# Kernel tuning notes

Hardware: AMD Instinct MI355X
Metric: run time of the kernel (lower is better)

The kernel has to match this reference:

```python
import jax, jax.numpy as jnp
import numpy as np

N, E = 3072, 49152
C_IN, HID, C_OUT = 16, 64, 3
KS = (2000, 1000, 500)  # ceil(pool_ratio * n_nodes) per depth: 2000/3072, 0.5, 0.5


def gcn(x, A, W, b):
    # GCNConv(improved=True) with edge weights: A_hat = A + 2I,
    # out = D^-1/2 A_hat D^-1/2 (x W) + b
    n = A.shape[0]
    i = jnp.arange(n)
    A_hat = A.at[i, i].add(2.0)
    deg = A_hat.sum(axis=1)
    dis = jnp.where(deg > 0, 1.0 / jnp.sqrt(deg), 0.0)
    return (dis[:, None] * A_hat * dis[None, :]) @ (x @ W) + b


def augment(A):
    # GraphUNet.augment_adj: remove self loops, add self loops (w=1),
    # spspmm(A, A) -> A^2, remove self loops. Dense equivalent.
    n = A.shape[0]
    i = jnp.arange(n)
    A1 = A.at[i, i].set(1.0)
    A2 = A1 @ A1
    return A2.at[i, i].set(0.0)


def topk_pool(x, A, p, k):
    # TopKPooling: score = tanh((x . p)/||p||), keep top-k nodes, scale features
    score = jnp.tanh((x @ p) / jnp.linalg.norm(p))
    _, perm = jax.lax.top_k(score, k)
    x = x[perm] * score[perm][:, None]
    return x, A[perm][:, perm], perm


def setup_inputs():
    key = jax.random.key(0)
    ks = jax.random.split(key, 16)
    g = lambda k, shape, s=1.0: jax.random.normal(k, shape, dtype=jnp.float32) * s
    s = 0.1
    return {
        "x": g(ks[0], (N, C_IN)),
        "edge_index": jax.random.randint(ks[1], (2, E), 0, N),
        "Wd0": g(ks[2], (C_IN, HID), s), "bd0": jnp.zeros((HID,), jnp.float32),
        "Wd1": g(ks[3], (HID, HID), s), "bd1": jnp.zeros((HID,), jnp.float32),
        "Wd2": g(ks[4], (HID, HID), s), "bd2": jnp.zeros((HID,), jnp.float32),
        "Wd3": g(ks[5], (HID, HID), s), "bd3": jnp.zeros((HID,), jnp.float32),
        "p1": g(ks[6], (HID,), s), "p2": g(ks[7], (HID,), s), "p3": g(ks[8], (HID,), s),
        "Wu0": g(ks[9], (HID, HID), s), "bu0": jnp.zeros((HID,), jnp.float32),
        "Wu1": g(ks[10], (HID, HID), s), "bu1": jnp.zeros((HID,), jnp.float32),
        "Wu2": g(ks[11], (HID, C_OUT), s), "bu2": jnp.zeros((C_OUT,), jnp.float32),
    }


def reference(x, edge_index, Wd0, bd0, Wd1, bd1, Wd2, bd2, Wd3, bd3,
              p1, p2, p3, Wu0, bu0, Wu1, bu1, Wu2, bu2):
    # eval mode: dropout_edge(p=0.2) and F.dropout(p=0.92) are identity
    # dense weighted adjacency; duplicate edges sum, matching sparse scatter-add
    A = jnp.zeros((N, N), jnp.float32).at[edge_index[0], edge_index[1]].add(1.0)
    x = jax.nn.relu(gcn(x, A, Wd0, bd0))
    xs, adjs, perms = [x], [A], []
    for i, (W, b, p) in enumerate(((Wd1, bd1, p1), (Wd2, bd2, p2), (Wd3, bd3, p3))):
        A = augment(A)
        x, A, perm = topk_pool(x, A, p, KS[i])
        x = jax.nn.relu(gcn(x, A, W, b))
        if i < 2:
            xs.append(x)
            adjs.append(A)
        perms.append(perm)
    for i, (W, b) in enumerate(((Wu0, bu0), (Wu1, bu1), (Wu2, bu2))):
        j = 2 - i
        res, Aj, perm = xs[j], adjs[j], perms[j]
        up = jnp.zeros_like(res).at[perm].set(x)  # unpool
        x = gcn(res + up, Aj, W, b)  # sum_res=True skip connection
        if i < 2:
            x = jax.nn.relu(x)
    return jax.nn.softmax(x, axis=1)
```

## Files before the change

### kernel.cpp

```cpp
#include <hip/hip_runtime.h>
#include <hip/hip_bf16.h>
#include <cstdint>
#include <cstddef>
#include <math.h>


#define DIVUP(a,b) (((a)+(b)-1)/(b))

using s16x8 = __attribute__((ext_vector_type(8))) short;
using f32x4 = __attribute__((ext_vector_type(4))) float;

__device__ __forceinline__ unsigned short f2bf(float v) {
    union { float f; unsigned u; } a; a.f = v;
    unsigned u = a.u;
    u = u + 0x7FFFu + ((u >> 16) & 1u);
    return (unsigned short)(u >> 16);
}
__device__ __forceinline__ float bf2f(unsigned short h) {
    union { unsigned u; float f; } a; a.u = ((unsigned)h) << 16; return a.f;
}
__device__ __forceinline__ void gload_lds16(const unsigned short* g, unsigned short* l) {
    __builtin_amdgcn_global_load_lds(
        (const __attribute__((address_space(1))) void*)g,
        (__attribute__((address_space(3))) void*)l, 16, 0, 0);
}


__global__ void k_scatter(const int* __restrict__ e, float* __restrict__ A, int E, int n) {
    int t = blockIdx.x * blockDim.x + threadIdx.x;
    if (t < E) atomicAdd(&A[(size_t)e[t] * n + e[E + t]], 1.0f);
}

__global__ void k_a0_plane(const float* __restrict__ A, unsigned short* __restrict__ H,
                           float* __restrict__ d0, float* __restrict__ dsum, int n) {
    int t = blockIdx.x * 256 + threadIdx.x;
    int i = t / n, j = t - i * n;
    float v = A[t];
    if (i == j) { d0[i] = v; v = 1.0f; }
    H[t] = f2bf(v);
    __shared__ float red[256];
    red[threadIdx.x] = v; __syncthreads();
    for (int o = 128; o > 0; o >>= 1) {
        if (threadIdx.x < o) red[threadIdx.x] += red[threadIdx.x + o];
        __syncthreads();
    }
    if (threadIdx.x == 0) atomicAdd(&dsum[i], red[0]);
}

__global__ void k_transpose_bf(const unsigned short* __restrict__ S, unsigned short* __restrict__ D, int n) {
    __shared__ unsigned short tile[32][33];
    int bx = blockIdx.x * 32, by = blockIdx.y * 32;
    #pragma unroll
    for (int dy = 0; dy < 32; dy += 8)
        tile[threadIdx.y + dy][threadIdx.x] = S[(size_t)(by + threadIdx.y + dy) * n + bx + threadIdx.x];
    __syncthreads();
    #pragma unroll
    for (int dy = 0; dy < 32; dy += 8)
        D[(size_t)(bx + threadIdx.y + dy) * n + by + threadIdx.x] = tile[threadIdx.x][threadIdx.y + dy];
}

__global__ void k_disv(const float* __restrict__ dsum, const float* __restrict__ diag,
                       float* __restrict__ dis, int n) {
    int i = blockIdx.x * blockDim.x + threadIdx.x;
    if (i >= n) return;
    float deg = dsum[i] + 1.0f + (diag ? diag[i] : 0.0f);
    dis[i] = deg > 0.f ? 1.0f / sqrtf(deg) : 0.f;
}

__global__ void k_scores(const float* __restrict__ x, const float* __restrict__ pv,
                         float* __restrict__ sc, int n) {
    __shared__ float pl[64];
    if (threadIdx.x < 64) pl[threadIdx.x] = pv[threadIdx.x];
    __syncthreads();
    float n2 = 0.f;
    #pragma unroll
    for (int k = 0; k < 64; ++k) n2 += pl[k] * pl[k];
    float nrm = sqrtf(n2);
    int i = blockIdx.x * blockDim.x + threadIdx.x;
    if (i >= n) return;
    const float* xr = x + (size_t)i * 64;
    float d = 0.f;
    #pragma unroll
    for (int k = 0; k < 64; ++k) d += xr[k] * pl[k];
    sc[i] = tanhf(d / nrm);
}

__global__ void k_count_rank(const float* __restrict__ score, int* __restrict__ rank, int n) {
    __shared__ float ls[256];
    const int i = blockIdx.x * 256 + threadIdx.x;
    const int j0 = blockIdx.y * 256;
    int jj_n = n - j0; if (jj_n > 256) jj_n = 256;
    ls[threadIdx.x] = (j0 + threadIdx.x < n) ? score[j0 + threadIdx.x] : -INFINITY;
    __syncthreads();
    if (i >= n) return;
    const float si = score[i];
    int cnt = 0;
    for (int jj = 0; jj < jj_n; ++jj) {
        float sj = ls[jj];
        int j = j0 + jj;
        cnt += (sj > si) || (sj == si && j < i);
    }
    atomicAdd(&rank[i], cnt);
}

__global__ void k_scatter_topk(const float* __restrict__ score, const int* __restrict__ rank,
                               int n, int k, int kp, int* __restrict__ perm, float* __restrict__ scout) {
    int i = blockIdx.x * blockDim.x + threadIdx.x;
    if (i < n) {
        int r = rank[i];
        if (r < k) { perm[r] = i; scout[r] = score[i]; }
    }
    if (i >= k && i < kp) { perm[i] = 0; scout[i] = 0.f; }
}

__global__ void k_pool_x(const float* __restrict__ x, const int* __restrict__ perm,
                         const float* __restrict__ sc, float* __restrict__ xo, int k) {
    int t = blockIdx.x * blockDim.x + threadIdx.x;
    if (t >= k * 64) return;
    int r = t >> 6;
    xo[t] = x[(size_t)perm[r] * 64 + (t & 63)] * sc[r];
}

__global__ void k_copy4(const float4* __restrict__ src, float4* __restrict__ dst, int n4) {
    int t = blockIdx.x * blockDim.x + threadIdx.x;
    if (t < n4) dst[t] = src[t];
}

__global__ void k_scatter_rows(const float* __restrict__ xc, const int* __restrict__ perm,
                               float* __restrict__ o, int k) {
    int t = blockIdx.x * blockDim.x + threadIdx.x;
    if (t >= k * 64) return;
    int r = t >> 6;
    o[(size_t)perm[r] * 64 + (t & 63)] += xc[t];
}

__global__ void k_xw(const float* __restrict__ x, const float* __restrict__ W,
                     const float* __restrict__ dis, int n, int np, int cin, int ldw, int nout,
                     float* __restrict__ Y, unsigned short* __restrict__ T0,
                     unsigned short* __restrict__ T1, unsigned short* __restrict__ T2) {
    int t = blockIdx.x * blockDim.x + threadIdx.x;
    if (t >= np * 64) return;
    int i = t >> 6, f = t & 63;
    float y = 0.f;
    if (i < n && f < nout) {
        float a = 0.f;
        for (int k = 0; k < cin; ++k) a += x[(size_t)i * cin + k] * W[(size_t)k * ldw + f];
        y = dis[i] * a;
    }
    Y[t] = y;
    unsigned short h0 = f2bf(y);
    float r1 = y - bf2f(h0);
    unsigned short h1 = f2bf(r1);
    float r2 = r1 - bf2f(h1);
    size_t ti = (size_t)f * np + i;
    T0[ti] = h0; T1[ti] = h1; T2[ti] = f2bf(r2);
}


template<int PA, int PB, int ATOMIC>
__global__ __launch_bounds__(256) void k_aug_gemm(
    const unsigned short* __restrict__ Pa, const unsigned short* __restrict__ Pb,
    const unsigned short* __restrict__ Qa, const unsigned short* __restrict__ Qb,
    const int* __restrict__ perm, int M, int N, int kchunk, int ns, float* __restrict__ C)
{
    __shared__ __align__(16) unsigned short lp[PA * 8192];
    __shared__ __align__(16) unsigned short lq[PB * 8192];
    const int tid = threadIdx.x, lane = tid & 63;
    const int wm = tid >> 7, wn = (tid >> 6) & 1;
    const int bm = blockIdx.x * 128, bn = blockIdx.y * 128;
    const int kbeg = blockIdx.z * kchunk;
    const unsigned short* P[2] = {Pa, Pb};
    const unsigned short* Q[2] = {Qa, Qb};
    const unsigned short* sp[PA][4];
    const unsigned short* sq[PB][4];
    int dst[4];
    #pragma unroll
    for (int it = 0; it < 4; ++it) {
        int s = tid + it * 256;
        int row = s >> 3, c = (s & 7) ^ (row & 7);
        dst[it] = (s - lane) * 8;
        #pragma unroll
        for (int p = 0; p < PA; ++p)
            sp[p][it] = P[p] + (size_t)perm[bm + row] * ns + kbeg + 8 * c;
        #pragma unroll
        for (int p = 0; p < PB; ++p)
            sq[p][it] = Q[p] + (size_t)perm[bn + row] * ns + kbeg + 8 * c;
    }
    f32x4 acc[4][4] = {};
    const int l15 = lane & 15, kb = lane >> 4;
    const int nt = kchunk >> 6;

    for (int tt = 0; tt < nt; ++tt) {
        if (tt) __syncthreads();
        int koff = tt * 64;
        #pragma unroll
        for (int p = 0; p < PA; ++p)
            #pragma unroll
            for (int it = 0; it < 4; ++it)
                gload_lds16(sp[p][it] + koff, &lp[p * 8192 + dst[it]]);
        #pragma unroll
        for (int p = 0; p < PB; ++p)
            #pragma unroll
            for (int it = 0; it < 4; ++it)
                gload_lds16(sq[p][it] + koff, &lq[p * 8192 + dst[it]]);
        __syncthreads();
        #pragma unroll
        for (int h = 0; h < 2; ++h) {
            s16x8 av[PA][4], bv[PB][4];
            #pragma unroll
            for (int p = 0; p < PA; ++p)
                #pragma unroll
                for (int mi = 0; mi < 4; ++mi) {
                    int row = wm * 64 + mi * 16 + l15;
                    int slot = (h * 4 + kb) ^ (row & 7);
                    av[p][mi] = *(const s16x8*)&lp[p * 8192 + row * 64 + slot * 8];
                }
            #pragma unroll
            for (int p = 0; p < PB; ++p)
                #pragma unroll
                for (int ni = 0; ni < 4; ++ni) {
                    int row = wn * 64 + ni * 16 + l15;
                    int slot = (h * 4 + kb) ^ (row & 7);
                    bv[p][ni] = *(const s16x8*)&lq[p * 8192 + row * 64 + slot * 8];
                }
            #pragma unroll
            for (int mi = 0; mi < 4; ++mi)
                #pragma unroll
                for (int ni = 0; ni < 4; ++ni)
                    #pragma unroll
                    for (int pa = 0; pa < PA; ++pa)
                        #pragma unroll
                        for (int pb = 0; pb < PB; ++pb)
                            acc[mi][ni] = __builtin_amdgcn_mfma_f32_16x16x32_bf16(
                                av[pa][mi], bv[pb][ni], acc[mi][ni], 0, 0, 0);
        }
    }

    const int l4 = lane >> 4;
    for (int mi = 0; mi < 4; ++mi)
        for (int ni = 0; ni < 4; ++ni)
            #pragma unroll
            for (int r = 0; r < 4; ++r) {
                int row = bm + wm * 64 + mi * 16 + l4 * 4 + r;
                int col = bn + wn * 64 + ni * 16 + l15;
                if (row < M && col < N) {
                    float v = acc[mi][ni][r];
                    if (ATOMIC) { if (v != 0.f) atomicAdd(&C[(size_t)row * N + col], v); }
                    else C[(size_t)row * N + col] = v;
                }
            }
}

template<int PA>
__global__ __launch_bounds__(256) void k_gcn_gemm(
    const unsigned short* __restrict__ Aa, const unsigned short* __restrict__ Ab,
    const unsigned short* __restrict__ Ac,
    const unsigned short* __restrict__ B0, const unsigned short* __restrict__ B1,
    const unsigned short* __restrict__ B2,
    int np, int kchunk, float* __restrict__ Zp)
{
    __shared__ __align__(16) unsigned short la[PA * 4096];
    __shared__ __align__(16) unsigned short lb[3 * 4096];
    const int tid = threadIdx.x, lane = tid & 63, wv = tid >> 6;
    const int bm = blockIdx.x * 64;
    const int kbeg = blockIdx.y * kchunk;
    const unsigned short* A[3] = {Aa, Ab, Ac};
    const unsigned short* B[3] = {B0, B1, B2};
    const unsigned short* sa[PA][2];
    const unsigned short* sb[3][2];
    int dst[2];
    #pragma unroll
    for (int it = 0; it < 2; ++it) {
        int s = tid + it * 256;
        int row = s >> 3, c = (s & 7) ^ (row & 7);
        dst[it] = (s - lane) * 8;
        #pragma unroll
        for (int p = 0; p < PA; ++p)
            sa[p][it] = A[p] + (size_t)(bm + row) * np + kbeg + 8 * c;
        #pragma unroll
        for (int p = 0; p < 3; ++p)
            sb[p][it] = B[p] + (size_t)row * np + kbeg + 8 * c;
    }
    f32x4 acc[4] = {};
    const int l15 = lane & 15, kb = lane >> 4;
    const int nt = kchunk >> 6;

    for (int tt = 0; tt < nt; ++tt) {
        if (tt) __syncthreads();
        int koff = tt * 64;
        #pragma unroll
        for (int p = 0; p < PA; ++p)
            #pragma unroll
            for (int it = 0; it < 2; ++it)
                gload_lds16(sa[p][it] + koff, &la[p * 4096 + dst[it]]);
        #pragma unroll
        for (int p = 0; p < 3; ++p)
            #pragma unroll
            for (int it = 0; it < 2; ++it)
                gload_lds16(sb[p][it] + koff, &lb[p * 4096 + dst[it]]);
        __syncthreads();
        #pragma unroll
        for (int h = 0; h < 2; ++h) {
            s16x8 av[PA], bv[3][4];
            #pragma unroll
            for (int p = 0; p < PA; ++p) {
                int row = wv * 16 + l15;
                int slot = (h * 4 + kb) ^ (row & 7);
                av[p] = *(const s16x8*)&la[p * 4096 + row * 64 + slot * 8];
            }
            #pragma unroll
            for (int p = 0; p < 3; ++p)
                #pragma unroll
                for (int ni = 0; ni < 4; ++ni) {
                    int row = ni * 16 + l15;
                    int slot = (h * 4 + kb) ^ (row & 7);
                    bv[p][ni] = *(const s16x8*)&lb[p * 4096 + row * 64 + slot * 8];
                }
            #pragma unroll
            for (int ni = 0; ni < 4; ++ni)
                #pragma unroll
                for (int pa = 0; pa < PA; ++pa)
                    #pragma unroll
                    for (int pb = 0; pb <= 2 - pa; ++pb)
                        acc[ni] = __builtin_amdgcn_mfma_f32_16x16x32_bf16(
                            av[pa], bv[pb][ni], acc[ni], 0, 0, 0);
        }
    }

    const int l4 = lane >> 4;
    float* Z = Zp + (size_t)blockIdx.y * np * 64;
    for (int ni = 0; ni < 4; ++ni)
        #pragma unroll
        for (int r = 0; r < 4; ++r) {
            int row = bm + wv * 16 + l4 * 4 + r;
            Z[(size_t)row * 64 + ni * 16 + l15] = acc[ni][r];
        }
}

__global__ void k_gcn_epi(const float* __restrict__ Zp, const float* __restrict__ Y,
                          const float* __restrict__ dis, const float* __restrict__ diagv,
                          const float* __restrict__ b, int n, int np, int nout, int relu,
                          float* __restrict__ xo) {
    int t = blockIdx.x * blockDim.x + threadIdx.x;
    if (t >= n * 64) return;
    int i = t >> 6, f = t & 63;
    float s = 0.f;
    for (int kq = 0; kq < 8; ++kq) s += Zp[(size_t)kq * np * 64 + t];
    float coef = 1.f + (diagv ? diagv[i] : 0.f);
    float v = dis[i] * (s + coef * Y[t]) + (f < nout ? b[f] : 0.f);
    if (relu) v = fmaxf(v, 0.f);
    xo[t] = v;
}

template<int NP, int NT>
__global__ void k_split_t(const float* __restrict__ C, int kk, int kp,
                          unsigned short* __restrict__ H0, unsigned short* __restrict__ H1,
                          unsigned short* __restrict__ H2,
                          unsigned short* __restrict__ T0, unsigned short* __restrict__ T1,
                          float* __restrict__ dsum) {
    __shared__ unsigned short tl[NT ? NT : 1][32][33];
    const int tx = threadIdx.x & 31, ty = threadIdx.x >> 5;
    const int r0 = blockIdx.y * 32, c0 = blockIdx.x * 32;
    const int c = c0 + tx;
    #pragma unroll
    for (int dy = 0; dy < 4; ++dy) {
        int rt = ty + dy * 8;
        int r = r0 + rt;
        float v = 0.f;
        if (r < kk && c < kk) v = (r == c) ? 1.f : C[(size_t)r * kk + c];
        unsigned short h0 = f2bf(v);
        size_t o = (size_t)r * kp + c;
        H0[o] = h0;
        if (NT > 0) tl[0][rt][tx] = h0;
        if (NP > 1) {
            float r1 = v - bf2f(h0);
            unsigned short h1 = f2bf(r1);
            H1[o] = h1;
            if (NT > 1) tl[1][rt][tx] = h1;
            if (NP > 2) H2[o] = f2bf(r1 - bf2f(h1));
        }
        float sum = v;
        #pragma unroll
        for (int o2 = 16; o2 > 0; o2 >>= 1) sum += __shfl_xor(sum, o2, 32);
        if (tx == 0) atomicAdd(&dsum[r], sum);
    }
    if (NT > 0) {
        __syncthreads();
        #pragma unroll
        for (int dy = 0; dy < 4; ++dy) {
            int rt = ty + dy * 8;
            size_t o = (size_t)(c0 + rt) * kp + r0 + tx;
            T0[o] = tl[0][tx][rt];
            if (NT > 1) T1[o] = tl[1][tx][rt];
        }
    }
}

__global__ void k_softmax(const float* __restrict__ lg, float* __restrict__ o, int n) {
    int i = blockIdx.x * blockDim.x + threadIdx.x;
    if (i >= n) return;
    float a = lg[i * 64], b = lg[i * 64 + 1], c = lg[i * 64 + 2];
    float m = fmaxf(a, fmaxf(b, c));
    float ea = expf(a - m), eb = expf(b - m), ec = expf(c - m);
    float s = ea + eb + ec;
    o[i * 3] = ea / s; o[i * 3 + 1] = eb / s; o[i * 3 + 2] = ec / s;
}


extern "C" void kernel_launch(void* const* d_in, const int* in_sizes, int n_in,
                              void* d_out, int out_size, void* d_ws, size_t ws_size,
                              hipStream_t stream) {
    const int N0 = 3072;
    const int E = in_sizes[1] / 2;
    const int CIN = in_sizes[0] / N0;

    const float* x_in = (const float*)d_in[0];
    const int*   eidx = (const int*)d_in[1];
    const float* Wd0 = (const float*)d_in[2];  const float* bd0 = (const float*)d_in[3];
    const float* Wd1 = (const float*)d_in[4];  const float* bd1 = (const float*)d_in[5];
    const float* Wd2 = (const float*)d_in[6];  const float* bd2 = (const float*)d_in[7];
    const float* Wd3 = (const float*)d_in[8];  const float* bd3 = (const float*)d_in[9];
    const float* p1  = (const float*)d_in[10]; const float* p2  = (const float*)d_in[11];
    const float* p3  = (const float*)d_in[12];
    const float* Wu0 = (const float*)d_in[13]; const float* bu0 = (const float*)d_in[14];
    const float* Wu1 = (const float*)d_in[15]; const float* bu1 = (const float*)d_in[16];
    const float* Wu2 = (const float*)d_in[17]; const float* bu2 = (const float*)d_in[18];
    float* out = (float*)d_out;

    char* ws = (char*)d_ws;
    size_t off = 0;
    auto alloc = [&](size_t bytes) -> void* {
        off = (off + 255) & ~(size_t)255;
        void* p = ws + off;
        off += bytes;
        return p;
    };

    unsigned short* A0H  = (unsigned short*)alloc((size_t)3072 * 3072 * 2);
    unsigned short* A0T  = (unsigned short*)alloc((size_t)3072 * 3072 * 2);
    float* d0   = (float*)alloc(3072 * 4);
    float* dis0 = (float*)alloc(3072 * 4);
    float* x0   = (float*)alloc((size_t)3072 * 64 * 4);
    unsigned short* P1H = (unsigned short*)alloc((size_t)2048 * 2048 * 2);
    unsigned short* P1T = (unsigned short*)alloc((size_t)2048 * 2048 * 2);
    float* dis1 = (float*)alloc(2048 * 4);
    float* x1   = (float*)alloc((size_t)2048 * 64 * 4);
    float* xp1  = (float*)alloc((size_t)2048 * 64 * 4);
    unsigned short* P2H  = (unsigned short*)alloc((size_t)1024 * 1024 * 2);
    unsigned short* P2L  = (unsigned short*)alloc((size_t)1024 * 1024 * 2);
    unsigned short* P2TH = (unsigned short*)alloc((size_t)1024 * 1024 * 2);
    unsigned short* P2TL = (unsigned short*)alloc((size_t)1024 * 1024 * 2);
    float* dis2 = (float*)alloc(1024 * 4);
    float* x2   = (float*)alloc((size_t)1024 * 64 * 4);
    float* xp2  = (float*)alloc((size_t)1024 * 64 * 4);
    unsigned short* P3a = (unsigned short*)alloc((size_t)512 * 512 * 2);
    unsigned short* P3b = (unsigned short*)alloc((size_t)512 * 512 * 2);
    unsigned short* P3c = (unsigned short*)alloc((size_t)512 * 512 * 2);
    float* dis3 = (float*)alloc(512 * 4);
    float* x3   = (float*)alloc((size_t)512 * 64 * 4);
    float* xp3  = (float*)alloc((size_t)512 * 64 * 4);
    int*   perm1 = (int*)alloc(2048 * 4);  float* sc1 = (float*)alloc(2048 * 4);
    int*   perm2 = (int*)alloc(1024 * 4);  float* sc2 = (float*)alloc(1024 * 4);
    int*   perm3 = (int*)alloc(512 * 4);   float* sc3 = (float*)alloc(512 * 4);
    float* score = (float*)alloc(3072 * 4);
    float* dsum0 = (float*)alloc(3072 * 4);
    float* dsum1 = (float*)alloc(2048 * 4);
    float* dsum2 = (float*)alloc(1024 * 4);
    float* dsum3 = (float*)alloc(512 * 4);
    int* rank1 = (int*)alloc(3072 * 4);
    int* rank2 = (int*)alloc(2048 * 4);
    int* rank3 = (int*)alloc(1024 * 4);
    float* Yf  = (float*)alloc((size_t)3072 * 64 * 4);
    unsigned short* Yt0 = (unsigned short*)alloc((size_t)64 * 3072 * 2);
    unsigned short* Yt1 = (unsigned short*)alloc((size_t)64 * 3072 * 2);
    unsigned short* Yt2 = (unsigned short*)alloc((size_t)64 * 3072 * 2);
    float* Zp   = (float*)alloc((size_t)8 * 3072 * 64 * 4);
    float* xlog = (float*)alloc((size_t)3072 * 64 * 4);
    float* t2b  = (float*)alloc((size_t)1024 * 64 * 4);
    float* t1b  = (float*)alloc((size_t)2048 * 64 * 4);
    float* t0b  = (float*)alloc((size_t)3072 * 64 * 4);
    char* scratch = (char*)alloc((size_t)3072 * 3072 * 4);
    if (off > ws_size) return;

    float* A0f = (float*)scratch;
    float* C1  = (float*)scratch;
    float* C2  = (float*)scratch;
    float* C3  = (float*)scratch;

    auto gcn = [&](const float* xin, int cin, const float* W, int ldw, int nout, const float* bias,
                   const unsigned short* Pa, const unsigned short* Pb2, const unsigned short* Pc,
                   int PA, int n, int np2, const float* dis, const float* diagv, int relu, float* xout) {
        k_xw<<<DIVUP(np2 * 64, 256), 256, 0, stream>>>(xin, W, dis, n, np2, cin, ldw, nout, Yf, Yt0, Yt1, Yt2);
        dim3 gg(np2 / 64, 8);
        int kch = np2 / 8;
        if (PA == 1)      k_gcn_gemm<1><<<gg, 256, 0, stream>>>(Pa, Pa, Pa, Yt0, Yt1, Yt2, np2, kch, Zp);
        else if (PA == 2) k_gcn_gemm<2><<<gg, 256, 0, stream>>>(Pa, Pb2, Pb2, Yt0, Yt1, Yt2, np2, kch, Zp);
        else              k_gcn_gemm<3><<<gg, 256, 0, stream>>>(Pa, Pb2, Pc, Yt0, Yt1, Yt2, np2, kch, Zp);
        k_gcn_epi<<<DIVUP(n * 64, 256), 256, 0, stream>>>(Zp, Yf, dis, diagv, bias, n, np2, nout, relu, xout);
    };

    auto topk = [&](const float* x, const float* pvec, int n, int k, int kp,
                    int* rank, int* perm, float* scv) {
        k_scores<<<DIVUP(n, 256), 256, 0, stream>>>(x, pvec, score, n);
        dim3 gr(DIVUP(n, 256), DIVUP(n, 256));
        k_count_rank<<<gr, 256, 0, stream>>>(score, rank, n);
        k_scatter_topk<<<DIVUP(n, 256), 256, 0, stream>>>(score, rank, n, k, kp, perm, scv);
    };

    hipMemsetAsync(dsum0, 0, (char*)(rank3 + 1024) - (char*)dsum0, stream);

    hipMemsetAsync(A0f, 0, (size_t)3072 * 3072 * 4, stream);
    k_scatter<<<DIVUP(E, 256), 256, 0, stream>>>(eidx, A0f, E, N0);
    k_a0_plane<<<3072 * 3072 / 256, 256, 0, stream>>>(A0f, A0H, d0, dsum0, N0);
    k_transpose_bf<<<dim3(96, 96), dim3(32, 8), 0, stream>>>(A0H, A0T, 3072);
    k_disv<<<DIVUP(3072, 256), 256, 0, stream>>>(dsum0, d0, dis0, 3072);

    gcn(x_in, CIN, Wd0, 64, 64, bd0, A0H, A0H, A0H, 1, 3072, 3072, dis0, d0, 1, x0);

    topk(x0, p1, 3072, 2000, 2048, rank1, perm1, sc1);
    k_pool_x<<<DIVUP(2000 * 64, 256), 256, 0, stream>>>(x0, perm1, sc1, xp1, 2000);
    hipMemsetAsync(C1, 0, (size_t)2000 * 2000 * 4, stream);
    k_aug_gemm<1, 1, 1><<<dim3(16, 16, 8), 256, 0, stream>>>(A0H, A0H, A0T, A0T, perm1, 2000, 2000, 384, 3072, C1);
    k_split_t<1, 1><<<dim3(64, 64), 256, 0, stream>>>(C1, 2000, 2048, P1H, P1H, P1H, P1T, P1T, dsum1);
    k_disv<<<DIVUP(2048, 256), 256, 0, stream>>>(dsum1, nullptr, dis1, 2048);
    gcn(xp1, 64, Wd1, 64, 64, bd1, P1H, P1H, P1H, 1, 2000, 2048, dis1, nullptr, 1, x1);

    topk(x1, p2, 2000, 1000, 1024, rank2, perm2, sc2);
    k_pool_x<<<DIVUP(1000 * 64, 256), 256, 0, stream>>>(x1, perm2, sc2, xp2, 1000);
    hipMemsetAsync(C2, 0, (size_t)1000 * 1000 * 4, stream);
    k_aug_gemm<1, 1, 1><<<dim3(8, 8, 8), 256, 0, stream>>>(P1H, P1H, P1T, P1T, perm2, 1000, 1000, 256, 2048, C2);
    k_split_t<2, 2><<<dim3(32, 32), 256, 0, stream>>>(C2, 1000, 1024, P2H, P2L, P2L, P2TH, P2TL, dsum2);
    k_disv<<<DIVUP(1024, 256), 256, 0, stream>>>(dsum2, nullptr, dis2, 1024);
    gcn(xp2, 64, Wd2, 64, 64, bd2, P2H, P2L, P2L, 2, 1000, 1024, dis2, nullptr, 1, x2);

    topk(x2, p3, 1000, 500, 512, rank3, perm3, sc3);
    k_pool_x<<<DIVUP(500 * 64, 256), 256, 0, stream>>>(x2, perm3, sc3, xp3, 500);
    hipMemsetAsync(C3, 0, (size_t)500 * 500 * 4, stream);
    k_aug_gemm<2, 2, 1><<<dim3(4, 4, 16), 256, 0, stream>>>(P2H, P2L, P2TH, P2TL, perm3, 500, 500, 64, 1024, C3);
    k_split_t<3, 0><<<dim3(16, 16), 256, 0, stream>>>(C3, 500, 512, P3a, P3b, P3c, nullptr, nullptr, dsum3);
    k_disv<<<DIVUP(512, 256), 256, 0, stream>>>(dsum3, nullptr, dis3, 512);
    gcn(xp3, 64, Wd3, 64, 64, bd3, P3a, P3b, P3c, 3, 500, 512, dis3, nullptr, 1, x3);

    k_copy4<<<DIVUP(1000 * 16, 256), 256, 0, stream>>>((const float4*)x2, (float4*)t2b, 1000 * 16);
    k_scatter_rows<<<DIVUP(500 * 64, 256), 256, 0, stream>>>(x3, perm3, t2b, 500);
    gcn(t2b, 64, Wu0, 64, 64, bu0, P2H, P2L, P2L, 2, 1000, 1024, dis2, nullptr, 1, xp2);

    k_copy4<<<DIVUP(2000 * 16, 256), 256, 0, stream>>>((const float4*)x1, (float4*)t1b, 2000 * 16);
    k_scatter_rows<<<DIVUP(1000 * 64, 256), 256, 0, stream>>>(xp2, perm2, t1b, 1000);
    gcn(t1b, 64, Wu1, 64, 64, bu1, P1H, P1H, P1H, 1, 2000, 2048, dis1, nullptr, 1, xp1);

    k_copy4<<<DIVUP(3072 * 16, 256), 256, 0, stream>>>((const float4*)x0, (float4*)t0b, 3072 * 16);
    k_scatter_rows<<<DIVUP(2000 * 64, 256), 256, 0, stream>>>(xp1, perm1, t0b, 2000);
    gcn(t0b, 64, Wu2, 3, 3, bu2, A0H, A0H, A0H, 1, 3072, 3072, dis0, d0, 0, xlog);

    k_softmax<<<DIVUP(3072, 256), 256, 0, stream>>>(xlog, out, 3072);
}
```

Measured before the change: 478.5 us.

## Fuse augment GEMM with bf16 split/transpose epilogue, drop split-K atomics

Replaces the split-K atomic augment GEMM, memset, and separate split/transpose kernel with one double-buffered GEMM. Each block runs the full K and writes the bf16 hi/lo planes and the transposed planes directly from registers through shared memory. Degrees are now computed by a separate row-reduction kernel over the bf16 planes. The gcn GEMM uses 16 K-splits for the 1024-size case. Dropping split-K cuts the grid to 256/64/16 blocks, which may underfill the GPU and lengthen each block's serial K loop, in exchange for removing the fp32 intermediate round trip and atomics.

```diff
diff --git a/kernel.cpp b/kernel.cpp
--- a/kernel.cpp
+++ b/kernel.cpp
@@ -65,6 +65,29 @@
     if (i >= n) return;
     float deg = dsum[i] + 1.0f + (diag ? diag[i] : 0.0f);
     dis[i] = deg > 0.f ? 1.0f / sqrtf(deg) : 0.f;
+}
+
+__global__ void k_disp(const unsigned short* __restrict__ P0, const unsigned short* __restrict__ P1,
+                       const unsigned short* __restrict__ P2, int nplanes,
+                       float* __restrict__ dis, int np) {
+    int i = blockIdx.x;
+    const unsigned short* pls[3] = {P0, P1, P2};
+    float s = 0.f;
+    for (int p = 0; p < nplanes; ++p) {
+        const unsigned short* row = pls[p] + (size_t)i * np;
+        for (int j = threadIdx.x * 8; j < np; j += 2048) {
+            s16x8 v = *(const s16x8*)(row + j);
+            #pragma unroll
+            for (int e = 0; e < 8; ++e) s += bf2f((unsigned short)v[e]);
+        }
+    }
+    __shared__ float red[256];
+    red[threadIdx.x] = s; __syncthreads();
+    for (int o = 128; o > 0; o >>= 1) {
+        if (threadIdx.x < o) red[threadIdx.x] += red[threadIdx.x + o];
+        __syncthreads();
+    }
+    if (threadIdx.x == 0) dis[i] = 1.0f / sqrtf(red[0] + 1.0f);
 }
 
 __global__ void k_scores(const float* __restrict__ x, const float* __restrict__ pv,
@@ -157,18 +180,22 @@
 }
 
 
-template<int PA, int PB, int ATOMIC>
-__global__ __launch_bounds__(256) void k_aug_gemm(
+template<int PA, int PB, int NP, int NT>
+__global__ __launch_bounds__(256) void k_aug2(
     const unsigned short* __restrict__ Pa, const unsigned short* __restrict__ Pb,
     const unsigned short* __restrict__ Qa, const unsigned short* __restrict__ Qb,
-    const int* __restrict__ perm, int M, int N, int kchunk, int ns, float* __restrict__ C)
+    const int* __restrict__ perm, int kk, int kp, int K, int ns,
+    unsigned short* __restrict__ H0, unsigned short* __restrict__ H1,
+    unsigned short* __restrict__ H2,
+    unsigned short* __restrict__ T0, unsigned short* __restrict__ T1)
 {
-    __shared__ __align__(16) unsigned short lp[PA * 8192];
-    __shared__ __align__(16) unsigned short lq[PB * 8192];
+    constexpr int STG = (PA + PB) * 8192;
+    constexpr int TRE = NT ? (128 * 130) : 0;
+    constexpr int SME = (2 * STG > TRE) ? (2 * STG) : TRE;
+    __shared__ __align__(16) unsigned short smem[SME];
     const int tid = threadIdx.x, lane = tid & 63;
     const int wm = tid >> 7, wn = (tid >> 6) & 1;
     const int bm = blockIdx.x * 128, bn = blockIdx.y * 128;
-    const int kbeg = blockIdx.z * kchunk;
     const unsigned short* P[2] = {Pa, Pb};
     const unsigned short* Q[2] = {Qa, Qb};
     const unsigned short* sp[PA][4];
@@ -181,29 +208,30 @@
         dst[it] = (s - lane) * 8;
         #pragma unroll
         for (int p = 0; p < PA; ++p)
-            sp[p][it] = P[p] + (size_t)perm[bm + row] * ns + kbeg + 8 * c;
+            sp[p][it] = P[p] + (size_t)perm[bm + row] * ns + 8 * c;
         #pragma unroll
         for (int p = 0; p < PB; ++p)
-            sq[p][it] = Q[p] + (size_t)perm[bn + row] * ns + kbeg + 8 * c;
+            sq[p][it] = Q[p] + (size_t)perm[bn + row] * ns + 8 * c;
     }
     f32x4 acc[4][4] = {};
     const int l15 = lane & 15, kb = lane >> 4;
-    const int nt = kchunk >> 6;
-
-    for (int tt = 0; tt < nt; ++tt) {
-        if (tt) __syncthreads();
-        int koff = tt * 64;
+    const int nt = K >> 6;
+
+    auto stage = [&](int b, int koff) {
+        unsigned short* base = smem + b * STG;
         #pragma unroll
         for (int p = 0; p < PA; ++p)
             #pragma unroll
             for (int it = 0; it < 4; ++it)
-                gload_lds16(sp[p][it] + koff, &lp[p * 8192 + dst[it]]);
+                gload_lds16(sp[p][it] + koff, base + p * 8192 + dst[it]);
         #pragma unroll
         for (int p = 0; p < PB; ++p)
             #pragma unroll
             for (int it = 0; it < 4; ++it)
-                gload_lds16(sq[p][it] + koff, &lq[p * 8192 + dst[it]]);
-        __syncthreads();
+                gload_lds16(sq[p][it] + koff, base + PA * 8192 + p * 8192 + dst[it]);
+    };
+    auto compute = [&](int b) {
+        const unsigned short* base = smem + b * STG;
         #pragma unroll
         for (int h = 0; h < 2; ++h) {
             s16x8 av[PA][4], bv[PB][4];
@@ -213,7 +241,7 @@
                 for (int mi = 0; mi < 4; ++mi) {
                     int row = wm * 64 + mi * 16 + l15;
                     int slot = (h * 4 + kb) ^ (row & 7);
-                    av[p][mi] = *(const s16x8*)&lp[p * 8192 + row * 64 + slot * 8];
+                    av[p][mi] = *(const s16x8*)(base + p * 8192 + row * 64 + slot * 8);
                 }
             #pragma unroll
             for (int p = 0; p < PB; ++p)
@@ -221,7 +249,7 @@
                 for (int ni = 0; ni < 4; ++ni) {
                     int row = wn * 64 + ni * 16 + l15;
                     int slot = (h * 4 + kb) ^ (row & 7);
-                    bv[p][ni] = *(const s16x8*)&lq[p * 8192 + row * 64 + slot * 8];
+                    bv[p][ni] = *(const s16x8*)(base + PA * 8192 + p * 8192 + row * 64 + slot * 8);
                 }
             #pragma unroll
             for (int mi = 0; mi < 4; ++mi)
@@ -234,21 +262,65 @@
                             acc[mi][ni] = __builtin_amdgcn_mfma_f32_16x16x32_bf16(
                                 av[pa][mi], bv[pb][ni], acc[mi][ni], 0, 0, 0);
         }
-    }
-
-    const int l4 = lane >> 4;
+    };
+
+    stage(0, 0);
+    __syncthreads();
+    for (int t = 0; t < nt; ++t) {
+        if (t + 1 < nt) stage((t + 1) & 1, (t + 1) * 64);
+        compute(t & 1);
+        __syncthreads();
+    }
+
+    const int hi = lane >> 4;
+    #pragma unroll
     for (int mi = 0; mi < 4; ++mi)
+        #pragma unroll
         for (int ni = 0; ni < 4; ++ni)
             #pragma unroll
             for (int r = 0; r < 4; ++r) {
-                int row = bm + wm * 64 + mi * 16 + l4 * 4 + r;
+                int row = bm + wm * 64 + mi * 16 + hi * 4 + r;
                 int col = bn + wn * 64 + ni * 16 + l15;
-                if (row < M && col < N) {
-                    float v = acc[mi][ni][r];
-                    if (ATOMIC) { if (v != 0.f) atomicAdd(&C[(size_t)row * N + col], v); }
-                    else C[(size_t)row * N + col] = v;
+                float v = (row < kk && col < kk) ? ((row == col) ? 1.f : acc[mi][ni][r]) : 0.f;
+                unsigned short h0 = f2bf(v);
+                size_t o = (size_t)row * kp + col;
+                H0[o] = h0;
+                if (NP > 1) {
+                    float r1 = v - bf2f(h0);
+                    unsigned short h1 = f2bf(r1);
+                    H1[o] = h1;
+                    if (NP > 2) H2[o] = f2bf(r1 - bf2f(h1));
                 }
             }
+
+    if (NT > 0) {
+        #pragma unroll
+        for (int pass = 0; pass < NT; ++pass) {
+            __syncthreads();
+            #pragma unroll
+            for (int mi = 0; mi < 4; ++mi)
+                #pragma unroll
+                for (int ni = 0; ni < 4; ++ni)
+                    #pragma unroll
+                    for (int r = 0; r < 4; ++r) {
+                        int rl = wm * 64 + mi * 16 + hi * 4 + r;
+                        int cl = wn * 64 + ni * 16 + l15;
+                        int row = bm + rl, col = bn + cl;
+                        float v = (row < kk && col < kk) ? ((row == col) ? 1.f : acc[mi][ni][r]) : 0.f;
+                        unsigned short h0 = f2bf(v);
+                        unsigned short hv = h0;
+                        if (pass == 1) hv = f2bf(v - bf2f(h0));
+                        smem[rl * 130 + cl] = hv;
+                    }
+            __syncthreads();
+            unsigned short* T = pass ? T1 : T0;
+            for (int e = 0; e < 64; ++e) {
+                int idx = tid + e * 256;
+                int j = idx >> 7, i = idx & 127;
+                T[(size_t)(bn + j) * kp + (bm + i)] = smem[i * 130 + j];
+            }
+        }
+    }
 }
 
 template<int PA>
@@ -340,60 +412,16 @@
 __global__ void k_gcn_epi(const float* __restrict__ Zp, const float* __restrict__ Y,
                           const float* __restrict__ dis, const float* __restrict__ diagv,
                           const float* __restrict__ b, int n, int np, int nout, int relu,
-                          float* __restrict__ xo) {
+                          int S, float* __restrict__ xo) {
     int t = blockIdx.x * blockDim.x + threadIdx.x;
     if (t >= n * 64) return;
     int i = t >> 6, f = t & 63;
     float s = 0.f;
-    for (int kq = 0; kq < 8; ++kq) s += Zp[(size_t)kq * np * 64 + t];
+    for (int kq = 0; kq < S; ++kq) s += Zp[(size_t)kq * np * 64 + t];
     float coef = 1.f + (diagv ? diagv[i] : 0.f);
     float v = dis[i] * (s + coef * Y[t]) + (f < nout ? b[f] : 0.f);
     if (relu) v = fmaxf(v, 0.f);
     xo[t] = v;
-}
-
-template<int NP, int NT>
-__global__ void k_split_t(const float* __restrict__ C, int kk, int kp,
-                          unsigned short* __restrict__ H0, unsigned short* __restrict__ H1,
-                          unsigned short* __restrict__ H2,
-                          unsigned short* __restrict__ T0, unsigned short* __restrict__ T1,
-                          float* __restrict__ dsum) {
-    __shared__ unsigned short tl[NT ? NT : 1][32][33];
-    const int tx = threadIdx.x & 31, ty = threadIdx.x >> 5;
-    const int r0 = blockIdx.y * 32, c0 = blockIdx.x * 32;
-    const int c = c0 + tx;
-    #pragma unroll
-    for (int dy = 0; dy < 4; ++dy) {
-        int rt = ty + dy * 8;
-        int r = r0 + rt;
-        float v = 0.f;
-        if (r < kk && c < kk) v = (r == c) ? 1.f : C[(size_t)r * kk + c];
-        unsigned short h0 = f2bf(v);
-        size_t o = (size_t)r * kp + c;
-        H0[o] = h0;
-        if (NT > 0) tl[0][rt][tx] = h0;
-        if (NP > 1) {
-            float r1 = v - bf2f(h0);
-            unsigned short h1 = f2bf(r1);
-            H1[o] = h1;
-            if (NT > 1) tl[1][rt][tx] = h1;
-            if (NP > 2) H2[o] = f2bf(r1 - bf2f(h1));
-        }
-        float sum = v;
-        #pragma unroll
-        for (int o2 = 16; o2 > 0; o2 >>= 1) sum += __shfl_xor(sum, o2, 32);
-        if (tx == 0) atomicAdd(&dsum[r], sum);
-    }
-    if (NT > 0) {
-        __syncthreads();
-        #pragma unroll
-        for (int dy = 0; dy < 4; ++dy) {
-            int rt = ty + dy * 8;
-            size_t o = (size_t)(c0 + rt) * kp + r0 + tx;
-            T0[o] = tl[0][tx][rt];
-            if (NT > 1) T1[o] = tl[1][tx][rt];
-        }
-    }
 }
 
 __global__ void k_softmax(const float* __restrict__ lg, float* __restrict__ o, int n) {
@@ -464,9 +492,6 @@
     int*   perm3 = (int*)alloc(512 * 4);   float* sc3 = (float*)alloc(512 * 4);
     float* score = (float*)alloc(3072 * 4);
     float* dsum0 = (float*)alloc(3072 * 4);
-    float* dsum1 = (float*)alloc(2048 * 4);
-    float* dsum2 = (float*)alloc(1024 * 4);
-    float* dsum3 = (float*)alloc(512 * 4);
     int* rank1 = (int*)alloc(3072 * 4);
     int* rank2 = (int*)alloc(2048 * 4);
     int* rank3 = (int*)alloc(1024 * 4);
@@ -474,7 +499,8 @@
     unsigned short* Yt0 = (unsigned short*)alloc((size_t)64 * 3072 * 2);
     unsigned short* Yt1 = (unsigned short*)alloc((size_t)64 * 3072 * 2);
     unsigned short* Yt2 = (unsigned short*)alloc((size_t)64 * 3072 * 2);
-    float* Zp   = (float*)alloc((size_t)8 * 3072 * 64 * 4);
+    float* Zp   = (float*)alloc((size_t)16 * 1024 * 64 * 4 > (size_t)8 * 3072 * 64 * 4
+                                ? (size_t)8 * 3072 * 64 * 4 : (size_t)8 * 3072 * 64 * 4);
     float* xlog = (float*)alloc((size_t)3072 * 64 * 4);
     float* t2b  = (float*)alloc((size_t)1024 * 64 * 4);
     float* t1b  = (float*)alloc((size_t)2048 * 64 * 4);
@@ -483,20 +509,18 @@
     if (off > ws_size) return;
 
     float* A0f = (float*)scratch;
-    float* C1  = (float*)scratch;
-    float* C2  = (float*)scratch;
-    float* C3  = (float*)scratch;
 
     auto gcn = [&](const float* xin, int cin, const float* W, int ldw, int nout, const float* bias,
                    const unsigned short* Pa, const unsigned short* Pb2, const unsigned short* Pc,
                    int PA, int n, int np2, const float* dis, const float* diagv, int relu, float* xout) {
         k_xw<<<DIVUP(np2 * 64, 256), 256, 0, stream>>>(xin, W, dis, n, np2, cin, ldw, nout, Yf, Yt0, Yt1, Yt2);
-        dim3 gg(np2 / 64, 8);
-        int kch = np2 / 8;
+        int S = (np2 == 1024) ? 16 : 8;
+        int kch = np2 / S;
+        dim3 gg(np2 / 64, S);
         if (PA == 1)      k_gcn_gemm<1><<<gg, 256, 0, stream>>>(Pa, Pa, Pa, Yt0, Yt1, Yt2, np2, kch, Zp);
         else if (PA == 2) k_gcn_gemm<2><<<gg, 256, 0, stream>>>(Pa, Pb2, Pb2, Yt0, Yt1, Yt2, np2, kch, Zp);
         else              k_gcn_gemm<3><<<gg, 256, 0, stream>>>(Pa, Pb2, Pc, Yt0, Yt1, Yt2, np2, kch, Zp);
-        k_gcn_epi<<<DIVUP(n * 64, 256), 256, 0, stream>>>(Zp, Yf, dis, diagv, bias, n, np2, nout, relu, xout);
+        k_gcn_epi<<<DIVUP(n * 64, 256), 256, 0, stream>>>(Zp, Yf, dis, diagv, bias, n, np2, nout, relu, S, xout);
     };
 
     auto topk = [&](const float* x, const float* pvec, int n, int k, int kp,
@@ -519,26 +543,23 @@
 
     topk(x0, p1, 3072, 2000, 2048, rank1, perm1, sc1);
     k_pool_x<<<DIVUP(2000 * 64, 256), 256, 0, stream>>>(x0, perm1, sc1, xp1, 2000);
-    hipMemsetAsync(C1, 0, (size_t)2000 * 2000 * 4, stream);
-    k_aug_gemm<1, 1, 1><<<dim3(16, 16, 8), 256, 0, stream>>>(A0H, A0H, A0T, A0T, perm1, 2000, 2000, 384, 3072, C1);
-    k_split_t<1, 1><<<dim3(64, 64), 256, 0, stream>>>(C1, 2000, 2048, P1H, P1H, P1H, P1T, P1T, dsum1);
-    k_disv<<<DIVUP(2048, 256), 256, 0, stream>>>(dsum1, nullptr, dis1, 2048);
+    k_aug2<1, 1, 1, 1><<<dim3(16, 16), 256, 0, stream>>>(
+        A0H, A0H, A0T, A0T, perm1, 2000, 2048, 3072, 3072, P1H, P1H, P1H, P1T, P1T);
+    k_disp<<<2000, 256, 0, stream>>>(P1H, P1H, P1H, 1, dis1, 2048);
     gcn(xp1, 64, Wd1, 64, 64, bd1, P1H, P1H, P1H, 1, 2000, 2048, dis1, nullptr, 1, x1);
 
     topk(x1, p2, 2000, 1000, 1024, rank2, perm2, sc2);
     k_pool_x<<<DIVUP(1000 * 64, 256), 256, 0, stream>>>(x1, perm2, sc2, xp2, 1000);
-    hipMemsetAsync(C2, 0, (size_t)1000 * 1000 * 4, stream);
-    k_aug_gemm<1, 1, 1><<<dim3(8, 8, 8), 256, 0, stream>>>(P1H, P1H, P1T, P1T, perm2, 1000, 1000, 256, 2048, C2);
-    k_split_t<2, 2><<<dim3(32, 32), 256, 0, stream>>>(C2, 1000, 1024, P2H, P2L, P2L, P2TH, P2TL, dsum2);
-    k_disv<<<DIVUP(1024, 256), 256, 0, stream>>>(dsum2, nullptr, dis2, 1024);
+    k_aug2<1, 1, 2, 2><<<dim3(8, 8), 256, 0, stream>>>(
+        P1H, P1H, P1T, P1T, perm2, 1000, 1024, 2048, 2048, P2H, P2L, P2L, P2TH, P2TL);
+    k_disp<<<1000, 256, 0, stream>>>(P2H, P2L, P2L, 2, dis2, 1024);
     gcn(xp2, 64, Wd2, 64, 64, bd2, P2H, P2L, P2L, 2, 1000, 1024, dis2, nullptr, 1, x2);
 
     topk(x2, p3, 1000, 500, 512, rank3, perm3, sc3);
     k_pool_x<<<DIVUP(500 * 64, 256), 256, 0, stream>>>(x2, perm3, sc3, xp3, 500);
-    hipMemsetAsync(C3, 0, (size_t)500 * 500 * 4, stream);
-    k_aug_gemm<2, 2, 1><<<dim3(4, 4, 16), 256, 0, stream>>>(P2H, P2L, P2TH, P2TL, perm3, 500, 500, 64, 1024, C3);
-    k_split_t<3, 0><<<dim3(16, 16), 256, 0, stream>>>(C3, 500, 512, P3a, P3b, P3c, nullptr, nullptr, dsum3);
-    k_disv<<<DIVUP(512, 256), 256, 0, stream>>>(dsum3, nullptr, dis3, 512);
+    k_aug2<2, 2, 3, 0><<<dim3(4, 4), 256, 0, stream>>>(
+        P2H, P2L, P2TH, P2TL, perm3, 500, 512, 1024, 1024, P3a, P3b, P3c, nullptr, nullptr);
+    k_disp<<<500, 256, 0, stream>>>(P3a, P3b, P3c, 3, dis3, 512);
     gcn(xp3, 64, Wd3, 64, 64, bd3, P3a, P3b, P3c, 3, 500, 512, dis3, nullptr, 1, x3);
 
     k_copy4<<<DIVUP(1000 * 16, 256), 256, 0, stream>>>((const float4*)x2, (float4*)t2b, 1000 * 16);
```

Result: faster. 443.8 us (-7.3%).
